# Kernel optimization log

Measured on AMD Instinct MI355X. Metric: run time of the kernel, lower is better.

Reference implementation:

```python
import jax, jax.numpy as jnp
import numpy as np

NUM_ACTIVE = 2  # top-k active experts

def setup_inputs() -> dict:
    key = jax.random.key(0)
    ks = jax.random.split(key, 5)
    B, N, D, H, E = 8192, 16, 128, 384, 8
    x = jax.random.normal(ks[0], (B, N, D), dtype=jnp.float32)
    # xavier-ish scales for stability
    router_w = jax.random.normal(ks[1], (E, N * D), dtype=jnp.float32) * (1.0 / np.sqrt(N * D))
    w1 = jax.random.normal(ks[2], (E, N, D, H), dtype=jnp.float32) * (1.0 / np.sqrt(D))
    w_gate = jax.random.normal(ks[3], (E, N, D, H), dtype=jnp.float32) * (1.0 / np.sqrt(D))
    w2 = jax.random.normal(ks[4], (E, N, H, D), dtype=jnp.float32) * (1.0 / np.sqrt(H))
    return {"x": x, "router_w": router_w, "w1": w1, "w_gate": w_gate, "w2": w2}

def reference(x, router_w, w1, w_gate, w2):
    B, N, D = x.shape
    E = w1.shape[0]
    # shared router over flattened heads
    router_logits = x.reshape(B, N * D) @ router_w.T            # (B, E)
    topk_logits, topk_idx = jax.lax.top_k(router_logits, NUM_ACTIVE)
    topk_w = jax.nn.softmax(topk_logits, axis=-1)               # (B, K)
    # combined routing weight per (token, expert); zero if expert not selected
    onehot = jax.nn.one_hot(topk_idx, E, dtype=x.dtype)         # (B, K, E)
    w_tok_exp = jnp.einsum('bk,bke->be', topk_w, onehot)        # (B, E)
    out = jnp.zeros_like(x)
    # loop over fixed, small expert count; unselected tokens get weight 0
    for e in range(E):
        h1 = jnp.einsum('bnd,ndh->bnh', x, w1[e])
        gate = jnp.einsum('bnd,ndh->bnh', x, w_gate[e])
        h = h1 * jax.nn.silu(gate)                              # SwiGLU (dropout=0 / eval)
        out_e = jnp.einsum('bnh,nhd->bnd', h, w2[e])
        out = out + w_tok_exp[:, e][:, None, None] * out_e
    return out
```

## Files before the change

kernel.cpp:

```cpp
#include <hip/hip_runtime.h>

#define NTOK  8192
#define NHEAD 16
#define DDIM  128
#define HDIM  384
#define NEXP  8
#define TILE  64
#define ENTRIES 2176

typedef __attribute__((ext_vector_type(8))) short short8;
typedef __attribute__((ext_vector_type(4))) float f32x4;

#define SZ_W1P   (8UL*16*4*24*512*2)
#define OFF_W1P  0UL
#define OFF_WGP  (OFF_W1P + SZ_W1P)
#define OFF_W2P  (OFF_WGP + SZ_W1P)
#define SZ_W2P   (8UL*16*12*8*512*2)
#define OFF_ROUT (OFF_W2P + SZ_W2P)
#define OFF_CNT  (OFF_ROUT + 8192UL*16)
#define OFF_TAB  (OFF_CNT + 256)
#define OFF_LIST (OFF_TAB + 2UL*ENTRIES*16)
#define OFF_WL   (OFF_LIST + 2UL*8192*4)

struct Routing { int i0, i1; float w0, w1; };

__device__ __forceinline__ unsigned short f2bf(float f) {
  unsigned int u = __float_as_uint(f);
  u += 0x7fffu + ((u >> 16) & 1u);
  return (unsigned short)(u >> 16);
}

__global__ __launch_bounds__(256) void convA_kernel(
    const float* __restrict__ w1, const float* __restrict__ wg,
    unsigned short* __restrict__ w1P, unsigned short* __restrict__ wgP) {
  __shared__ float ls[32][388];
  const int kk = blockIdx.x;
  const int en = blockIdx.y;
  const float* src = (blockIdx.z == 0 ? w1 : wg) + ((size_t)en * DDIM + kk * 32) * HDIM;
  unsigned short* dst = (blockIdx.z == 0 ? w1P : wgP) + ((size_t)en * 4 + kk) * (24 * 512);
  const int tid = threadIdx.x;
  #pragma unroll
  for (int i = 0; i < 12; ++i) {
    int f4 = i * 256 + tid;
    int row = f4 / 96, c4 = f4 % 96;
    float4 v = reinterpret_cast<const float4*>(src + (size_t)row * HDIM)[c4];
    ls[row][c4*4+0] = v.x; ls[row][c4*4+1] = v.y;
    ls[row][c4*4+2] = v.z; ls[row][c4*4+3] = v.w;
  }
  __syncthreads();
  #pragma unroll
  for (int i = 0; i < 6; ++i) {
    int fid = i * 256 + tid;
    int ct = fid >> 6, lane = fid & 63;
    int r0 = (lane >> 4) * 8, c = ct * 16 + (lane & 15);
    unsigned short o[8];
    #pragma unroll
    for (int j = 0; j < 8; ++j) o[j] = f2bf(ls[r0 + j][c]);
    reinterpret_cast<uint4*>(dst + (size_t)(ct * 64 + lane) * 8)[0] =
        make_uint4((unsigned)o[0] | ((unsigned)o[1] << 16),
                   (unsigned)o[2] | ((unsigned)o[3] << 16),
                   (unsigned)o[4] | ((unsigned)o[5] << 16),
                   (unsigned)o[6] | ((unsigned)o[7] << 16));
  }
}

__global__ __launch_bounds__(256) void convB_kernel(
    const float* __restrict__ w2, unsigned short* __restrict__ w2P) {
  __shared__ float ls[32][132];
  const int kk = blockIdx.x;
  const int en = blockIdx.y;
  const float* src = w2 + ((size_t)en * HDIM + kk * 32) * DDIM;
  unsigned short* dst = w2P + ((size_t)en * 12 + kk) * (8 * 512);
  const int tid = threadIdx.x;
  #pragma unroll
  for (int i = 0; i < 4; ++i) {
    int f4 = i * 256 + tid;
    int row = f4 >> 5, c4 = f4 & 31;
    float4 v = reinterpret_cast<const float4*>(src + (size_t)row * DDIM)[c4];
    ls[row][c4*4+0] = v.x; ls[row][c4*4+1] = v.y;
    ls[row][c4*4+2] = v.z; ls[row][c4*4+3] = v.w;
  }
  __syncthreads();
  #pragma unroll
  for (int i = 0; i < 2; ++i) {
    int fid = i * 256 + tid;
    int ct = fid >> 6, lane = fid & 63;
    int r0 = (lane >> 4) * 8, c = ct * 16 + (lane & 15);
    unsigned short o[8];
    #pragma unroll
    for (int j = 0; j < 8; ++j) o[j] = f2bf(ls[r0 + j][c]);
    reinterpret_cast<uint4*>(dst + (size_t)(ct * 64 + lane) * 8)[0] =
        make_uint4((unsigned)o[0] | ((unsigned)o[1] << 16),
                   (unsigned)o[2] | ((unsigned)o[3] << 16),
                   (unsigned)o[4] | ((unsigned)o[5] << 16),
                   (unsigned)o[6] | ((unsigned)o[7] << 16));
  }
}

__global__ __launch_bounds__(256) void router_kernel(
    const float* __restrict__ x, const float* __restrict__ rw,
    Routing* __restrict__ routing) {
  const int lane = threadIdx.x & 63;
  const int wgid = blockIdx.x * 4 + (threadIdx.x >> 6);
  const int tok0 = wgid * 4;
  float acc[4][8];
  #pragma unroll
  for (int t = 0; t < 4; ++t)
    #pragma unroll
    for (int e = 0; e < 8; ++e) acc[t][e] = 0.f;
  const float4* xr = reinterpret_cast<const float4*>(x);
  const float4* wr = reinterpret_cast<const float4*>(rw);
  #pragma unroll
  for (int c = 0; c < 8; ++c) {
    float4 wv[8];
    #pragma unroll
    for (int e = 0; e < 8; ++e) wv[e] = wr[e * 512 + c * 64 + lane];
    #pragma unroll
    for (int t = 0; t < 4; ++t) {
      float4 xv = xr[(size_t)(tok0 + t) * 512 + c * 64 + lane];
      #pragma unroll
      for (int e = 0; e < 8; ++e)
        acc[t][e] += xv.x * wv[e].x + xv.y * wv[e].y + xv.z * wv[e].z + xv.w * wv[e].w;
    }
  }
  #pragma unroll
  for (int t = 0; t < 4; ++t)
    #pragma unroll
    for (int e = 0; e < 8; ++e) {
      acc[t][e] += __shfl_xor(acc[t][e], 1);
      acc[t][e] += __shfl_xor(acc[t][e], 2);
      acc[t][e] += __shfl_xor(acc[t][e], 4);
    }
  const int l3 = lane & 7;
  #pragma unroll
  for (int t = 0; t < 4; ++t) {
    float v0 = (l3 & 1) ? acc[t][1] : acc[t][0];
    float v1 = (l3 & 1) ? acc[t][3] : acc[t][2];
    float v2 = (l3 & 1) ? acc[t][5] : acc[t][4];
    float v3 = (l3 & 1) ? acc[t][7] : acc[t][6];
    float u0 = (l3 & 2) ? v1 : v0;
    float u1 = (l3 & 2) ? v3 : v2;
    float sel = (l3 & 4) ? u1 : u0;
    sel += __shfl_xor(sel, 8);
    sel += __shfl_xor(sel, 16);
    sel += __shfl_xor(sel, 32);
    float le[8];
    #pragma unroll
    for (int e = 0; e < 8; ++e) le[e] = __shfl(sel, e);
    if (lane == 0) {
      int tok = tok0 + t;
      int i0 = 0; float m0 = le[0];
      #pragma unroll
      for (int e = 1; e < 8; ++e) if (le[e] > m0) { m0 = le[e]; i0 = e; }
      int i1 = -1; float m1 = -3.4e38f;
      #pragma unroll
      for (int e = 0; e < 8; ++e) if (e != i0 && le[e] > m1) { m1 = le[e]; i1 = e; }
      float ed = __expf(m1 - m0);
      Routing r; r.i0 = i0; r.i1 = i1;
      r.w0 = 1.f / (1.f + ed); r.w1 = ed / (1.f + ed);
      routing[tok] = r;
    }
  }
}

__global__ __launch_bounds__(256) void count_kernel(
    const Routing* __restrict__ routing, int* __restrict__ cnt) {
  const int s = blockIdx.x >> 3, e = blockIdx.x & 7;
  const int tid = threadIdx.x;
  int c = 0;
  for (int t = tid; t < NTOK; t += 256) {
    Routing r = routing[t];
    c += ((s == 0 ? r.i0 : r.i1) == e);
  }
  c += __shfl_xor(c, 32); c += __shfl_xor(c, 16); c += __shfl_xor(c, 8);
  c += __shfl_xor(c, 4);  c += __shfl_xor(c, 2);  c += __shfl_xor(c, 1);
  __shared__ int wsum[4];
  if ((tid & 63) == 0) wsum[tid >> 6] = c;
  __syncthreads();
  if (tid == 0) cnt[blockIdx.x] = wsum[0] + wsum[1] + wsum[2] + wsum[3];
}

__global__ void build_kernel(const int* __restrict__ cnt, int* __restrict__ cur,
                             int4* __restrict__ table) {
  const int tid = threadIdx.x;
  for (int i = tid; i < 2 * ENTRIES; i += 256)
    table[i] = make_int4(0, 0, 0, 0);
  __syncthreads();
  if (tid < 16) {
    int s = tid >> 3, e = tid & 7;
    int base = 0;
    for (int k = 0; k < e; ++k) base += cnt[s * 8 + k];
    cur[tid] = base;
  }
  __syncthreads();
  if (tid < 16) {
    int s = tid >> 3, xcd = tid & 7;
    int j = 0;
    int base = 0;
    for (int e = 0; e < 8; ++e) {
      int c = cnt[s * 8 + e];
      #pragma unroll
      for (int nn = 0; nn < 2; ++nn) {
        int n = xcd + nn * 8;
        for (int t = 0; t < c; t += TILE) {
          int rc = c - t; if (rc > TILE) rc = TILE;
          table[s * ENTRIES + xcd + 8 * j] = make_int4(e, base + t, rc, n);
          ++j;
        }
      }
      base += c;
    }
  }
}

__global__ __launch_bounds__(256) void compact_kernel(
    const Routing* __restrict__ routing, const int* __restrict__ cur,
    int* __restrict__ list, float* __restrict__ wl) {
  const int s = blockIdx.x >> 3, e = blockIdx.x & 7;
  const int tid = threadIdx.x;
  __shared__ int ps[256];
  int myc = 0;
  for (int t = tid; t < NTOK; t += 256) {
    Routing r = routing[t];
    myc += ((s == 0 ? r.i0 : r.i1) == e);
  }
  ps[tid] = myc;
  __syncthreads();
  for (int off = 1; off < 256; off <<= 1) {
    int v = (tid >= off) ? ps[tid - off] : 0;
    __syncthreads();
    ps[tid] += v;
    __syncthreads();
  }
  int base = cur[blockIdx.x] + ps[tid] - myc;
  for (int t = tid; t < NTOK; t += 256) {
    Routing r = routing[t];
    int ei = (s == 0 ? r.i0 : r.i1);
    if (ei == e) {
      list[s * NTOK + base] = t;
      wl[s * NTOK + base] = (s == 0 ? r.w0 : r.w1);
      ++base;
    }
  }
}

__global__ __launch_bounds__(256, 4) void expert_kernel(
    const float* __restrict__ x,
    const unsigned short* __restrict__ w1P,
    const unsigned short* __restrict__ wgP,
    const unsigned short* __restrict__ w2P,
    const int* __restrict__ list, const float* __restrict__ wl,
    const int4* __restrict__ table,
    float* __restrict__ out, const int slot)
{
  extern __shared__ char smem[];
  char* xs = smem;
  char* Pb = smem + 16384;
  const int4 tb = table[slot * ENTRIES + blockIdx.x];
  const int e = tb.x, rbeg = tb.y, rcnt = tb.z, n = tb.w;
  if (rcnt == 0) return;
  const int* lst = list + slot * NTOK + rbeg;
  const float* wls = wl + slot * NTOK + rbeg;
  const int tid = threadIdx.x;

  {
    const int cpos = tid & 31;
    const int rsub = tid >> 5;
    #pragma unroll
    for (int it = 0; it < 8; ++it) {
      int row = it * 8 + rsub;
      unsigned int lo = 0, hi = 0;
      if (row < rcnt) {
        int tok = lst[row];
        float4 v = reinterpret_cast<const float4*>(x + ((size_t)tok * NHEAD + n) * DDIM)[cpos];
        lo = (unsigned)f2bf(v.x) | ((unsigned)f2bf(v.y) << 16);
        hi = (unsigned)f2bf(v.z) | ((unsigned)f2bf(v.w) << 16);
      }
      int byte = row * 256 + ((cpos * 8) ^ ((row & 7) << 4));
      *reinterpret_cast<uint2*>(xs + byte) = make_uint2(lo, hi);
    }
  }
  __syncthreads();

  const int wid = tid >> 6, lane = tid & 63;
  const int lr = lane & 15, lq = lane >> 4;
  char* pw = Pb + wid * 1536;
  const f32x4 z4 = {0.f, 0.f, 0.f, 0.f};

  short8 a[4];
  #pragma unroll
  for (int kk = 0; kk < 4; ++kk) {
    int row = wid * 16 + lr;
    int byte = row * 256 + (((kk * 32 + lq * 8) * 2) ^ ((row & 7) << 4));
    a[kk] = *reinterpret_cast<const short8*>(xs + byte);
  }

  f32x4 acc[8];
  #pragma unroll
  for (int ct = 0; ct < 8; ++ct) acc[ct] = z4;

  const unsigned short* w1b = w1P + (size_t)(e * NHEAD + n) * (4 * 24 * 512);
  const unsigned short* wgb = wgP + (size_t)(e * NHEAD + n) * (4 * 24 * 512);
  const unsigned short* w2b = w2P + (size_t)(e * NHEAD + n) * (12 * 8 * 512);

  for (int c = 0; c < 12; ++c) {
    #pragma unroll
    for (int ct2 = 0; ct2 < 2; ++ct2) {
      const int ctg = c * 2 + ct2;
      f32x4 ah = z4, ag = z4;
      #pragma unroll
      for (int kk = 0; kk < 4; ++kk) {
        short8 b1 = *reinterpret_cast<const short8*>(w1b + ((size_t)(kk * 24 + ctg) * 64 + lane) * 8);
        short8 bg = *reinterpret_cast<const short8*>(wgb + ((size_t)(kk * 24 + ctg) * 64 + lane) * 8);
        ah = __builtin_amdgcn_mfma_f32_16x16x32_bf16(a[kk], b1, ah, 0, 0, 0);
        ag = __builtin_amdgcn_mfma_f32_16x16x32_bf16(a[kk], bg, ag, 0, 0, 0);
      }
      #pragma unroll
      for (int r = 0; r < 4; ++r) {
        float h1 = ah[r], g = ag[r];
        float val = h1 * g * __builtin_amdgcn_rcpf(1.f + __expf(-g));
        int row = lq * 4 + r;
        int hl = ct2 * 16 + lr;
        *reinterpret_cast<unsigned short*>(pw + row * 80 + hl * 2) = f2bf(val);
      }
    }
    short8 a2 = *reinterpret_cast<const short8*>(pw + lr * 80 + lq * 16);
    #pragma unroll
    for (int ct = 0; ct < 8; ++ct) {
      short8 b = *reinterpret_cast<const short8*>(w2b + ((size_t)(c * 8 + ct) * 64 + lane) * 8);
      acc[ct] = __builtin_amdgcn_mfma_f32_16x16x32_bf16(a2, b, acc[ct], 0, 0, 0);
    }
  }

  #pragma unroll
  for (int r = 0; r < 4; ++r) {
    int lrow = wid * 16 + lq * 4 + r;
    if (lrow < rcnt) {
      int tok = lst[lrow];
      float wt = wls[lrow];
      float* op = out + ((size_t)tok * NHEAD + n) * DDIM;
      #pragma unroll
      for (int ct = 0; ct < 8; ++ct) {
        int col = ct * 16 + lr;
        float v = acc[ct][r] * wt;
        if (slot == 0) op[col] = v;
        else          op[col] += v;
      }
    }
  }
}

extern "C" void kernel_launch(void* const* d_in, const int* in_sizes, int n_in,
                              void* d_out, int out_size, void* d_ws, size_t ws_size,
                              hipStream_t stream) {
  const float* x  = (const float*)d_in[0];
  const float* rw = (const float*)d_in[1];
  const float* w1 = (const float*)d_in[2];
  const float* wg = (const float*)d_in[3];
  const float* w2 = (const float*)d_in[4];
  float* out = (float*)d_out;
  char* ws = (char*)d_ws;

  unsigned short* w1P = (unsigned short*)(ws + OFF_W1P);
  unsigned short* wgP = (unsigned short*)(ws + OFF_WGP);
  unsigned short* w2P = (unsigned short*)(ws + OFF_W2P);
  Routing* routing = (Routing*)(ws + OFF_ROUT);
  int* cnt = (int*)(ws + OFF_CNT);
  int* cur = cnt + 16;
  int4* table = (int4*)(ws + OFF_TAB);
  int* list = (int*)(ws + OFF_LIST);
  float* wl = (float*)(ws + OFF_WL);

  convA_kernel<<<dim3(4, 128, 2), 256, 0, stream>>>(w1, wg, w1P, wgP);
  convB_kernel<<<dim3(12, 128, 1), 256, 0, stream>>>(w2, w2P);
  router_kernel<<<512, 256, 0, stream>>>(x, rw, routing);
  count_kernel<<<16, 256, 0, stream>>>(routing, cnt);
  build_kernel<<<1, 256, 0, stream>>>(cnt, cur, table);
  compact_kernel<<<16, 256, 0, stream>>>(routing, cur, list, wl);
  expert_kernel<<<ENTRIES, 256, 22528, stream>>>(
      x, w1P, wgP, w2P, list, wl, table, out, 0);
  expert_kernel<<<ENTRIES, 256, 22528, stream>>>(
      x, w1P, wgP, w2P, list, wl, table, out, 1);
}
```

Before: 299.8 us.

## Double-buffer expert weight fragments in registers to overlap loads with MFMA

Restructures the expert FFN inner loop so the W1/Wgate fragments for the next 16-column hidden tile, and the W2 fragments, are loaded into a two-slot register buffer while MFMAs run on the current slot. The 12-iteration chunk loop is fully unrolled and the two sub-tiles are written out explicitly, so buffer indices are resolved at compile time. The aim is to hide global-memory load latency behind matrix work. In exchange, register pressure rises, and launch bounds are relaxed from 4 to 3 blocks per CU, which may lower occupancy.

```diff
diff --git a/kernel.cpp b/kernel.cpp
--- a/kernel.cpp
+++ b/kernel.cpp
@@ -244,7 +244,7 @@
   }
 }
 
-__global__ __launch_bounds__(256, 4) void expert_kernel(
+__global__ __launch_bounds__(256, 3) void expert_kernel(
     const float* __restrict__ x,
     const unsigned short* __restrict__ w1P,
     const unsigned short* __restrict__ wgP,
@@ -303,32 +303,69 @@
   const unsigned short* wgb = wgP + (size_t)(e * NHEAD + n) * (4 * 24 * 512);
   const unsigned short* w2b = w2P + (size_t)(e * NHEAD + n) * (12 * 8 * 512);
 
+  short8 bw[2][8];
+
+  #pragma unroll
+  for (int kk = 0; kk < 4; ++kk) {
+    bw[0][kk]     = *reinterpret_cast<const short8*>(w1b + ((size_t)(kk * 24 + 0) * 64 + lane) * 8);
+    bw[0][kk + 4] = *reinterpret_cast<const short8*>(wgb + ((size_t)(kk * 24 + 0) * 64 + lane) * 8);
+  }
+
+  #pragma unroll
   for (int c = 0; c < 12; ++c) {
-    #pragma unroll
-    for (int ct2 = 0; ct2 < 2; ++ct2) {
-      const int ctg = c * 2 + ct2;
+    const int p0 = c & 1;
+    const int p1 = p0 ^ 1;
+
+    #pragma unroll
+    for (int kk = 0; kk < 4; ++kk) {
+      bw[p1][kk]     = *reinterpret_cast<const short8*>(w1b + ((size_t)(kk * 24 + 2 * c + 1) * 64 + lane) * 8);
+      bw[p1][kk + 4] = *reinterpret_cast<const short8*>(wgb + ((size_t)(kk * 24 + 2 * c + 1) * 64 + lane) * 8);
+    }
+    {
       f32x4 ah = z4, ag = z4;
       #pragma unroll
       for (int kk = 0; kk < 4; ++kk) {
-        short8 b1 = *reinterpret_cast<const short8*>(w1b + ((size_t)(kk * 24 + ctg) * 64 + lane) * 8);
-        short8 bg = *reinterpret_cast<const short8*>(wgb + ((size_t)(kk * 24 + ctg) * 64 + lane) * 8);
-        ah = __builtin_amdgcn_mfma_f32_16x16x32_bf16(a[kk], b1, ah, 0, 0, 0);
-        ag = __builtin_amdgcn_mfma_f32_16x16x32_bf16(a[kk], bg, ag, 0, 0, 0);
+        ah = __builtin_amdgcn_mfma_f32_16x16x32_bf16(a[kk], bw[p0][kk],     ah, 0, 0, 0);
+        ag = __builtin_amdgcn_mfma_f32_16x16x32_bf16(a[kk], bw[p0][kk + 4], ag, 0, 0, 0);
       }
       #pragma unroll
       for (int r = 0; r < 4; ++r) {
         float h1 = ah[r], g = ag[r];
         float val = h1 * g * __builtin_amdgcn_rcpf(1.f + __expf(-g));
-        int row = lq * 4 + r;
-        int hl = ct2 * 16 + lr;
-        *reinterpret_cast<unsigned short*>(pw + row * 80 + hl * 2) = f2bf(val);
-      }
-    }
-    short8 a2 = *reinterpret_cast<const short8*>(pw + lr * 80 + lq * 16);
-    #pragma unroll
-    for (int ct = 0; ct < 8; ++ct) {
-      short8 b = *reinterpret_cast<const short8*>(w2b + ((size_t)(c * 8 + ct) * 64 + lane) * 8);
-      acc[ct] = __builtin_amdgcn_mfma_f32_16x16x32_bf16(a2, b, acc[ct], 0, 0, 0);
+        *reinterpret_cast<unsigned short*>(pw + (lq * 4 + r) * 80 + lr * 2) = f2bf(val);
+      }
+    }
+
+    #pragma unroll
+    for (int ct = 0; ct < 8; ++ct)
+      bw[p0][ct] = *reinterpret_cast<const short8*>(w2b + ((size_t)(c * 8 + ct) * 64 + lane) * 8);
+    {
+      f32x4 ah = z4, ag = z4;
+      #pragma unroll
+      for (int kk = 0; kk < 4; ++kk) {
+        ah = __builtin_amdgcn_mfma_f32_16x16x32_bf16(a[kk], bw[p1][kk],     ah, 0, 0, 0);
+        ag = __builtin_amdgcn_mfma_f32_16x16x32_bf16(a[kk], bw[p1][kk + 4], ag, 0, 0, 0);
+      }
+      #pragma unroll
+      for (int r = 0; r < 4; ++r) {
+        float h1 = ah[r], g = ag[r];
+        float val = h1 * g * __builtin_amdgcn_rcpf(1.f + __expf(-g));
+        *reinterpret_cast<unsigned short*>(pw + (lq * 4 + r) * 80 + (16 + lr) * 2) = f2bf(val);
+      }
+    }
+
+    if (c < 11) {
+      #pragma unroll
+      for (int kk = 0; kk < 4; ++kk) {
+        bw[p1][kk]     = *reinterpret_cast<const short8*>(w1b + ((size_t)(kk * 24 + 2 * c + 2) * 64 + lane) * 8);
+        bw[p1][kk + 4] = *reinterpret_cast<const short8*>(wgb + ((size_t)(kk * 24 + 2 * c + 2) * 64 + lane) * 8);
+      }
+    }
+    {
+      short8 a2 = *reinterpret_cast<const short8*>(pw + lr * 80 + lq * 16);
+      #pragma unroll
+      for (int ct = 0; ct < 8; ++ct)
+        acc[ct] = __builtin_amdgcn_mfma_f32_16x16x32_bf16(a2, bw[p0][ct], acc[ct], 0, 0, 0);
     }
   }
 
```

Result: slower. 313.8 us (+4.7%).
